# Performance work log

Measured on AMD Instinct MI355X. Metric: run time of the kernel, lower is better.

The kernel has to match this reference:

```python
import jax, jax.numpy as jnp
import numpy as np

N, E, H, L, T = 20000, 160000, 128, 4, 20


def _ln(x, g, b):
    m = jnp.mean(x, -1, keepdims=True)
    v = jnp.mean((x - m) ** 2, -1, keepdims=True)
    return (x - m) * jax.lax.rsqrt(v + 1e-5) * g + b


def _mlp(x, W1, b1, W2, b2, g, b):
    # Linear -> ReLU -> Linear -> LayerNorm, as in mlp_2layer
    h = jax.nn.relu(x @ W1 + b1)
    return _ln(h @ W2 + b2, g, b)


def setup_inputs() -> dict:
    key = jax.random.key(0)
    ks = iter(jax.random.split(key, 64))

    def W(shape):
        fan_in = shape[-2]
        return jax.random.normal(next(ks), shape, jnp.float32) * (fan_in ** -0.5)

    z = lambda s: jnp.zeros(s, jnp.float32)
    o = lambda s: jnp.ones(s, jnp.float32)

    inp = {
        'x': jax.random.normal(next(ks), (N, 12), jnp.float32),
        'edge_attr': jax.random.normal(next(ks), (E, 4), jnp.float32),
        'edge_index': jax.random.randint(next(ks), (2, E), 0, N),
        # node encoder (12 -> H)
        'Wn1': W((12, H)), 'bn1': z((H,)), 'Wn2': W((H, H)), 'bn2': z((H,)), 'gn_ln': o((H,)), 'bn_ln': z((H,)),
        # edge encoder (4 -> H)
        'We1': W((4, H)), 'be1': z((H,)), 'We2': W((H, H)), 'be2': z((H,)), 'ge_ln': o((H,)), 'be_ln': z((H,)),
        # stacked per-layer params: edge_mlp (4H -> H), node_mlp (3H -> H), global_mlp (3H -> H)
        'lEW1': W((L, 4 * H, H)), 'lEb1': z((L, H)), 'lEW2': W((L, H, H)), 'lEb2': z((L, H)), 'lEg': o((L, H)), 'lEbt': z((L, H)),
        'lVW1': W((L, 3 * H, H)), 'lVb1': z((L, H)), 'lVW2': W((L, H, H)), 'lVb2': z((L, H)), 'lVg': o((L, H)), 'lVbt': z((L, H)),
        'lGW1': W((L, 3 * H, H)), 'lGb1': z((L, H)), 'lGW2': W((L, H, H)), 'lGb2': z((L, H)), 'lGg': o((L, H)), 'lGbt': z((L, H)),
        # CNN output head: Conv1d(1->8,k=15,s=4) -> ReLU -> Conv1d(8->1,k=10,s=1)
        'c1w': jax.random.normal(next(ks), (8, 1, 15), jnp.float32) * 0.1, 'c1b': z((8,)),
        'c2w': jax.random.normal(next(ks), (1, 8, 10), jnp.float32) * 0.1, 'c2b': z((1,)),
    }
    return inp


def _forward(x, edge_attr, edge_index,
             Wn1, bn1, Wn2, bn2, gn_ln, bn_ln,
             We1, be1, We2, be2, ge_ln, be_ln,
             lEW1, lEb1, lEW2, lEb2, lEg, lEbt,
             lVW1, lVb1, lVW2, lVb2, lVg, lVbt,
             lGW1, lGb1, lGW2, lGb2, lGg, lGbt,
             c1w, c1b, c2w, c2b):
    senders = edge_index[0]
    receivers = edge_index[1]
    n_nodes = x.shape[0]
    n_edges = edge_attr.shape[0]

    x_v = _mlp(x, Wn1, bn1, Wn2, bn2, gn_ln, bn_ln)          # [N, H]
    x_e = _mlp(edge_attr, We1, be1, We2, be2, ge_ln, be_ln)  # [E, H]
    g = jnp.zeros((1, H), x_v.dtype)                          # B=1 global (no global inputs)

    def step(carry, p):
        x_v, x_e, g = carry
        (EW1, Eb1, EW2, Eb2, Eg, Ebt,
         VW1, Vb1, VW2, Vb2, Vg, Vbt,
         GW1, Gb1, GW2, Gb2, Gg, Gbt) = p
        # edge update: gather sender/receiver feats, concat with edge + global
        g_e = jnp.broadcast_to(g, (n_edges, H))
        edge_in = jnp.concatenate([x_v[senders], x_v[receivers], x_e, g_e], -1)  # [E, 4H]
        x_e = x_e + _mlp(edge_in, EW1, Eb1, EW2, Eb2, Eg, Ebt)
        # node update: sum-aggregate messages by receiver
        aggr = jax.ops.segment_sum(x_e, receivers, num_segments=n_nodes)  # [N, H]
        g_v = jnp.broadcast_to(g, (n_nodes, H))
        node_in = jnp.concatenate([x_v, aggr, g_v], -1)  # [N, 3H]
        x_v = x_v + _mlp(node_in, VW1, Vb1, VW2, Vb2, Vg, Vbt)
        # global update
        g_in = jnp.concatenate([jnp.sum(x_v, 0, keepdims=True), jnp.sum(x_e, 0, keepdims=True), g], -1)  # [1, 3H]
        g = g + _mlp(g_in, GW1, Gb1, GW2, Gb2, Gg, Gbt)
        return (x_v, x_e, g), None

    params = (lEW1, lEb1, lEW2, lEb2, lEg, lEbt,
              lVW1, lVb1, lVW2, lVb2, lVg, lVbt,
              lGW1, lGb1, lGW2, lGb2, lGg, lGbt)
    (x_v, x_e, g), _ = jax.lax.scan(step, (x_v, x_e, g), params)

    # CNN head over the H=128 feature axis -> [N, T]
    dn = ('NCH', 'OIH', 'NCH')
    h = x_v[:, None, :]  # [N, 1, 128]
    h = jax.lax.conv_general_dilated(h, c1w, (4,), 'VALID', dimension_numbers=dn)
    h = jax.nn.relu(h + c1b[None, :, None])  # [N, 8, 29]
    h = jax.lax.conv_general_dilated(h, c2w, (1,), 'VALID', dimension_numbers=dn) + c2b[None, :, None]
    return h[:, 0, :]  # [N, 20]


def reference(x, edge_attr, edge_index,
              Wn1, bn1, Wn2, bn2, gn_ln, bn_ln,
              We1, be1, We2, be2, ge_ln, be_ln,
              lEW1, lEb1, lEW2, lEb2, lEg, lEbt,
              lVW1, lVb1, lVW2, lVb2, lVg, lVbt,
              lGW1, lGb1, lGW2, lGb2, lGg, lGbt,
              c1w, c1b, c2w, c2b):
    return _forward(x, edge_attr, edge_index,
                    Wn1, bn1, Wn2, bn2, gn_ln, bn_ln,
                    We1, be1, We2, be2, ge_ln, be_ln,
                    lEW1, lEb1, lEW2, lEb2, lEg, lEbt,
                    lVW1, lVb1, lVW2, lVb2, lVg, lVbt,
                    lGW1, lGb1, lGW2, lGb2, lGg, lGbt,
                    c1w, c1b, c2w, c2b)
```

## Files before the change

### kernel.cpp

```cpp
#include <hip/hip_runtime.h>

#define NN 20000
#define NE 160000
#define HD 128
#define SA 136

typedef __attribute__((ext_vector_type(8))) short  bfrag;
typedef __attribute__((ext_vector_type(4))) short  s4v;
typedef __attribute__((ext_vector_type(4))) float  facc;
typedef __attribute__((ext_vector_type(4))) float  f4v;

__device__ __forceinline__ float bf2f(unsigned short u){
  union { unsigned int i; float f; } v; v.i = ((unsigned int)u) << 16; return v.f;
}
__device__ __forceinline__ unsigned short f2bf(float f){
  union { float f; unsigned int i; } v; v.f = f;
  unsigned int r = v.i + 0x7fffu + ((v.i >> 16) & 1u);
  return (unsigned short)(r >> 16);
}

__global__ void sentinel_kernel(float* out, float code){
  if (threadIdx.x < 32) out[threadIdx.x] = code;
}

__device__ __forceinline__ void gemm_tile(const short* Ab,
                                          const unsigned short* pk,
                                          int m0, int lane, facc acc[8]){
  const int q = lane >> 4, c = lane & 15;
  #pragma unroll
  for (int kt = 0; kt < 4; ++kt){
    bfrag a = *(const bfrag*)(Ab + (m0 + c) * SA + kt * 32 + q * 8);
    const bfrag* bp = (const bfrag*)pk + kt * 512 + lane;
    #pragma unroll
    for (int nt = 0; nt < 8; ++nt){
      acc[nt] = __builtin_amdgcn_mfma_f32_16x16x32_bf16(a, bp[nt * 64], acc[nt], 0, 0, 0);
    }
  }
}

__device__ __forceinline__ void gemm_tile_h(const short* Ab,
                                            const unsigned short* pk,
                                            int m0, int ntb, int lane, facc acc[4]){
  const int q = lane >> 4, c = lane & 15;
  #pragma unroll
  for (int kt = 0; kt < 4; ++kt){
    bfrag a = *(const bfrag*)(Ab + (m0 + c) * SA + kt * 32 + q * 8);
    const bfrag* bp = (const bfrag*)pk + kt * 512 + ntb * 64 + lane;
    #pragma unroll
    for (int nt = 0; nt < 4; ++nt){
      acc[nt] = __builtin_amdgcn_mfma_f32_16x16x32_bf16(a, bp[nt * 64], acc[nt], 0, 0, 0);
    }
  }
}

__global__ __launch_bounds__(256) void pack_all(
    const float* Wn2, const float* We2,
    const float* lEW1, const float* lEW2,
    const float* lVW1, const float* lVW2,
    unsigned short* packed)
{
  int job = blockIdx.x * 256 + threadIdx.x;
  int mat = job >> 12, r12 = job & 4095;
  int plane = r12 >> 11, r = r12 & 2047;
  int kt = r >> 9, nt = (r >> 6) & 7, lane = r & 63;
  const float* src;
  if (mat == 0) src = Wn2;
  else if (mat == 1) src = We2;
  else {
    int m2 = mat - 2, l = m2 / 7, t = m2 % 7;
    switch (t){
      case 0: src = lEW1 + ((size_t)l*512 +   0)*HD; break;
      case 1: src = lEW1 + ((size_t)l*512 + 128)*HD; break;
      case 2: src = lEW1 + ((size_t)l*512 + 256)*HD; break;
      case 3: src = lEW2 + (size_t)l*HD*HD;          break;
      case 4: src = lVW1 + ((size_t)l*384 +   0)*HD; break;
      case 5: src = lVW1 + ((size_t)l*384 + 128)*HD; break;
      default: src = lVW2 + (size_t)l*HD*HD;         break;
    }
  }
  int krow = kt*32 + (lane>>4)*8, col = nt*16 + (lane&15);
  unsigned short v[8];
  #pragma unroll
  for (int j = 0; j < 8; ++j){
    float w = src[(size_t)(krow + j)*HD + col];
    unsigned short h = f2bf(w);
    v[j] = plane ? f2bf(w - bf2f(h)) : h;
  }
  unsigned short* dst = packed + ((size_t)mat*2 + plane)*16384
                               + ((size_t)(kt*8+nt)*64 + lane)*8;
  #pragma unroll
  for (int j = 0; j < 8; ++j) dst[j] = v[j];
}

__global__ __launch_bounds__(128) void init_small(
    float* g, float* cbe, float* cbv, float* xvs, float* xes,
    const float* Eb1_0, const float* Vb1_0)
{
  int t = threadIdx.x;
  g[t] = 0.f; xvs[t] = 0.f; xes[t] = 0.f;
  cbe[t] = Eb1_0[t]; cbv[t] = Vb1_0[t];
}

__global__ __launch_bounds__(256) void zero_cnt(int* cnt){
  int i = blockIdx.x * 256 + threadIdx.x;
  if (i < NN) cnt[i] = 0;
}
__global__ __launch_bounds__(256) void hist_kernel(const int* eidx, int* cnt){
  int e = blockIdx.x * 256 + threadIdx.x;
  atomicAdd(&cnt[eidx[NE + e]], 1);
}
__global__ __launch_bounds__(1024) void scan_kernel(const int* cnt, int* base, int* ofs){
  __shared__ int wsum[16];
  int t = threadIdx.x, lane = t & 63;
  int vals[20]; int loc = 0;
  if (t < 1000){
    #pragma unroll
    for (int k = 0; k < 20; ++k){ vals[k] = cnt[t*20 + k]; loc += vals[k]; }
  }
  int inc = loc;
  #pragma unroll
  for (int d = 1; d < 64; d <<= 1){ int o = __shfl_up(inc, d); if (lane >= d) inc += o; }
  if (lane == 63) wsum[t >> 6] = inc;
  __syncthreads();
  if (t < 16){
    int v = wsum[t];
    #pragma unroll
    for (int d = 1; d < 16; d <<= 1){ int o = __shfl_up(v, d); if (t >= d) v += o; }
    wsum[t] = v;
  }
  __syncthreads();
  int woff = (t >= 64) ? wsum[(t >> 6) - 1] : 0;
  int run = woff + inc - loc;
  if (t < 1000){
    #pragma unroll
    for (int k = 0; k < 20; ++k){ base[t*20 + k] = run; ofs[t*20 + k] = run; run += vals[k]; }
  }
  if (t == 0) base[NN] = NE;
}
__global__ __launch_bounds__(256) void scatter_kernel(const int* eidx, int* ofs,
                                                      int* perm, int* ssid, int* srid){
  int e = blockIdx.x * 256 + threadIdx.x;
  int s = eidx[e], r = eidx[NE + e];
  int pos = atomicAdd(&ofs[r], 1);
  perm[pos] = e; ssid[pos] = s; srid[pos] = r;
}

__global__ __launch_bounds__(256) void enc_node(
    const float* x, const float* W1, const float* b1,
    const unsigned short* pkW2, const float* b2,
    const float* gl, const float* bl, float* xvf, int nrows)
{
  __shared__ float inb[64*12];
  __shared__ __align__(16) short Hh[64*SA];
  __shared__ __align__(16) short Hl[64*SA];
  int tid = threadIdx.x, r0 = blockIdx.x * 64;
  for (int j = tid; j < 64*12; j += 256){
    int rr = j / 12, k = j % 12, rg = r0 + rr;
    inb[j] = (rg < nrows) ? x[(size_t)rg*12 + k] : 0.f;
  }
  __syncthreads();
  {
    int cc = tid & 127;
    float w1c[12];
    #pragma unroll
    for (int k = 0; k < 12; ++k) w1c[k] = W1[k*HD + cc];
    float bb = b1[cc];
    for (int it = 0; it < 32; ++it){
      int rr = it*2 + (tid >> 7);
      float a = bb;
      #pragma unroll
      for (int k = 0; k < 12; ++k) a += inb[rr*12 + k] * w1c[k];
      float h = fmaxf(a, 0.f);
      unsigned short hh = f2bf(h);
      Hh[rr*SA + cc] = (short)hh;
      Hl[rr*SA + cc] = (short)f2bf(h - bf2f(hh));
    }
  }
  __syncthreads();
  int lane = tid & 63, q = lane >> 4, c = lane & 15, m0 = (tid >> 6) * 16;
  facc a2[8];
  #pragma unroll
  for (int nt = 0; nt < 8; ++nt) a2[nt] = (facc){0.f,0.f,0.f,0.f};
  gemm_tile(Hh, pkW2,         m0, lane, a2);
  gemm_tile(Hl, pkW2,         m0, lane, a2);
  gemm_tile(Hh, pkW2 + 16384, m0, lane, a2);
  #pragma unroll
  for (int i = 0; i < 4; ++i){
    int rl = m0 + q*4 + i, rg = r0 + rl;
    float vals[8], s = 0.f, ss = 0.f;
    #pragma unroll
    for (int nt = 0; nt < 8; ++nt){
      float v = a2[nt][i] + b2[nt*16 + c];
      vals[nt] = v; s += v; ss += v*v;
    }
    s += __shfl_xor(s,1); ss += __shfl_xor(ss,1);
    s += __shfl_xor(s,2); ss += __shfl_xor(ss,2);
    s += __shfl_xor(s,4); ss += __shfl_xor(ss,4);
    s += __shfl_xor(s,8); ss += __shfl_xor(ss,8);
    float mean = s * 0.0078125f;
    float var  = ss * 0.0078125f - mean*mean;
    float rs   = rsqrtf(var + 1e-5f);
    if (rg < nrows){
      #pragma unroll
      for (int nt = 0; nt < 8; ++nt){
        int col = nt*16 + c;
        xvf[(size_t)rg*HD + col] = (vals[nt]-mean)*rs*gl[col] + bl[col];
      }
    }
  }
}

__global__ __launch_bounds__(256) void enc_edge(
    const float* ea, const int* perm, const float* W1, const float* b1,
    const unsigned short* pkW2, const float* b2,
    const float* gl, const float* bl, unsigned short* xeb)
{
  __shared__ float inb[64*4];
  __shared__ __align__(16) short Hh[64*SA];
  __shared__ __align__(16) short Hl[64*SA];
  int tid = threadIdx.x, r0 = blockIdx.x * 64;
  {
    int rr = tid >> 2, k = tid & 3;
    int pe = perm[r0 + rr];
    inb[tid] = ea[(size_t)pe*4 + k];
  }
  __syncthreads();
  {
    int cc = tid & 127;
    float w0 = W1[0*HD+cc], w1 = W1[1*HD+cc], w2 = W1[2*HD+cc], w3 = W1[3*HD+cc];
    float bb = b1[cc];
    for (int it = 0; it < 32; ++it){
      int rr = it*2 + (tid >> 7);
      float a = bb + inb[rr*4+0]*w0 + inb[rr*4+1]*w1 + inb[rr*4+2]*w2 + inb[rr*4+3]*w3;
      float h = fmaxf(a, 0.f);
      unsigned short hh = f2bf(h);
      Hh[rr*SA + cc] = (short)hh;
      Hl[rr*SA + cc] = (short)f2bf(h - bf2f(hh));
    }
  }
  __syncthreads();
  int lane = tid & 63, q = lane >> 4, c = lane & 15, m0 = (tid >> 6) * 16;
  facc a2[8];
  #pragma unroll
  for (int nt = 0; nt < 8; ++nt) a2[nt] = (facc){0.f,0.f,0.f,0.f};
  gemm_tile(Hh, pkW2,         m0, lane, a2);
  gemm_tile(Hl, pkW2,         m0, lane, a2);
  gemm_tile(Hh, pkW2 + 16384, m0, lane, a2);
  #pragma unroll
  for (int i = 0; i < 4; ++i){
    int rl = m0 + q*4 + i, rg = r0 + rl;
    float vals[8], s = 0.f, ss = 0.f;
    #pragma unroll
    for (int nt = 0; nt < 8; ++nt){
      float v = a2[nt][i] + b2[nt*16 + c];
      vals[nt] = v; s += v; ss += v*v;
    }
    s += __shfl_xor(s,1); ss += __shfl_xor(ss,1);
    s += __shfl_xor(s,2); ss += __shfl_xor(ss,2);
    s += __shfl_xor(s,4); ss += __shfl_xor(ss,4);
    s += __shfl_xor(s,8); ss += __shfl_xor(ss,8);
    float mean = s * 0.0078125f;
    float var  = ss * 0.0078125f - mean*mean;
    float rs   = rsqrtf(var + 1e-5f);
    #pragma unroll
    for (int nt = 0; nt < 8; ++nt){
      int col = nt*16 + c;
      xeb[(size_t)rg*HD + col] = f2bf((vals[nt]-mean)*rs*gl[col] + bl[col]);
    }
  }
}

__global__ __launch_bounds__(512, 4) void pq_kernel(
    const float* xvf, const unsigned short* pkA, const unsigned short* pkB,
    unsigned short* P, unsigned short* Q, int nrows)
{
  __shared__ __align__(16) short Ah[64*SA];
  __shared__ __align__(16) short Al[64*SA];
  int tid = threadIdx.x, r0 = blockIdx.x * 64;
  for (int j = tid; j < 1024; j += 512){
    int rr = j >> 4, ch = j & 15, rg = r0 + rr;
    float v[8];
    if (rg < nrows){
      f4v a = *(const f4v*)(xvf + (size_t)rg*HD + ch*8);
      f4v b = *(const f4v*)(xvf + (size_t)rg*HD + ch*8 + 4);
      v[0]=a[0];v[1]=a[1];v[2]=a[2];v[3]=a[3];v[4]=b[0];v[5]=b[1];v[6]=b[2];v[7]=b[3];
    } else {
      #pragma unroll
      for (int k = 0; k < 8; ++k) v[k] = 0.f;
    }
    short* dh = Ah + rr*SA + ch*8;
    short* dl = Al + rr*SA + ch*8;
    #pragma unroll
    for (int k = 0; k < 8; ++k){
      unsigned short h = f2bf(v[k]);
      dh[k] = (short)h; dl[k] = (short)f2bf(v[k] - bf2f(h));
    }
  }
  __syncthreads();
  int lane = tid & 63, wq = tid >> 6, q = lane >> 4, c = lane & 15;
  int m0 = (wq & 3) * 16, ntb = (wq >> 2) * 4;
  facc ap[4], aq[4];
  #pragma unroll
  for (int nt = 0; nt < 4; ++nt){ ap[nt] = (facc){0.f,0.f,0.f,0.f}; aq[nt] = (facc){0.f,0.f,0.f,0.f}; }
  gemm_tile_h(Ah, pkA,         m0, ntb, lane, ap);
  gemm_tile_h(Al, pkA,         m0, ntb, lane, ap);
  gemm_tile_h(Ah, pkA + 16384, m0, ntb, lane, ap);
  gemm_tile_h(Ah, pkB,         m0, ntb, lane, aq);
  gemm_tile_h(Al, pkB,         m0, ntb, lane, aq);
  gemm_tile_h(Ah, pkB + 16384, m0, ntb, lane, aq);
  #pragma unroll
  for (int i = 0; i < 4; ++i){
    int rl = m0 + q*4 + i, rg = r0 + rl;
    if (rg < nrows){
      s4v pv, qv;
      #pragma unroll
      for (int nt = 0; nt < 4; ++nt){
        pv[nt] = (short)f2bf(ap[nt][i]);
        qv[nt] = (short)f2bf(aq[nt][i]);
      }
      *(s4v*)(P + (size_t)rg*HD + c*8 + ntb) = pv;
      *(s4v*)(Q + (size_t)rg*HD + c*8 + ntb) = qv;
    }
  }
}

__global__ __launch_bounds__(512, 4) void edge_kernel(
    unsigned short* xeb, const int* ssid, const int* srid,
    const unsigned short* P, const unsigned short* Q, const float* cbe,
    const unsigned short* pkW1c, const unsigned short* pkW2,
    const float* Eb2, const float* Eg, const float* Ebt)
{
  __shared__ __align__(16) short Ab[64*SA];
  __shared__ __align__(16) short Hl[64*SA];
  __shared__ int sidx[64], ridx[64];
  __shared__ float lnS[128], lnSS[128];
  int tid = threadIdx.x, e0 = blockIdx.x * 64;
  for (int j = tid; j < 1024; j += 512){
    int rr = j >> 4, ch = j & 15;
    *(bfrag*)(Ab + rr*SA + ch*8) = *(const bfrag*)(xeb + (size_t)(e0+rr)*HD + ch*8);
  }
  if (tid < 64){ sidx[tid] = ssid[e0+tid]; ridx[tid] = srid[e0+tid]; }
  __syncthreads();
  int lane = tid & 63, wq = tid >> 6, q = lane >> 4, c = lane & 15;
  int m0 = (wq & 3) * 16, ntb = (wq >> 2) * 4, half = wq >> 2;
  unsigned int rres[4][2];
  #pragma unroll
  for (int i = 0; i < 4; ++i){
    int rl = m0 + q*4 + i;
    #pragma unroll
    for (int p2 = 0; p2 < 2; ++p2){
      unsigned short a0 = (unsigned short)Ab[rl*SA + (ntb + 2*p2    )*16 + c];
      unsigned short a1 = (unsigned short)Ab[rl*SA + (ntb + 2*p2 + 1)*16 + c];
      rres[i][p2] = ((unsigned int)a1 << 16) | a0;
    }
  }
  float cb[4];
  #pragma unroll
  for (int nt = 0; nt < 4; ++nt) cb[nt] = cbe[(ntb + nt)*16 + c];
  float pg[4][4];
  #pragma unroll
  for (int i = 0; i < 4; ++i){
    int rl = m0 + q*4 + i;
    s4v ps = *(const s4v*)(P + (size_t)sidx[rl]*HD + c*8 + ntb);
    s4v qr = *(const s4v*)(Q + (size_t)ridx[rl]*HD + c*8 + ntb);
    #pragma unroll
    for (int nt = 0; nt < 4; ++nt)
      pg[i][nt] = bf2f((unsigned short)ps[nt]) + bf2f((unsigned short)qr[nt]) + cb[nt];
  }
  facc acc[4];
  #pragma unroll
  for (int nt = 0; nt < 4; ++nt) acc[nt] = (facc){0.f,0.f,0.f,0.f};
  gemm_tile_h(Ab, pkW1c,         m0, ntb, lane, acc);
  gemm_tile_h(Ab, pkW1c + 16384, m0, ntb, lane, acc);
  __syncthreads();
  #pragma unroll
  for (int i = 0; i < 4; ++i){
    int rl = m0 + q*4 + i;
    #pragma unroll
    for (int nt = 0; nt < 4; ++nt){
      int col = (ntb + nt)*16 + c;
      float h = fmaxf(acc[nt][i] + pg[i][nt], 0.f);
      unsigned short hh = f2bf(h);
      Ab[rl*SA + col] = (short)hh;
      Hl[rl*SA + col] = (short)f2bf(h - bf2f(hh));
    }
  }
  __syncthreads();
  facc a2[4];
  #pragma unroll
  for (int nt = 0; nt < 4; ++nt) a2[nt] = (facc){0.f,0.f,0.f,0.f};
  gemm_tile_h(Ab, pkW2,         m0, ntb, lane, a2);
  gemm_tile_h(Hl, pkW2,         m0, ntb, lane, a2);
  gemm_tile_h(Ab, pkW2 + 16384, m0, ntb, lane, a2);
  float vals[4][4], myS[4], mySS[4];
  #pragma unroll
  for (int i = 0; i < 4; ++i){
    int rl = m0 + q*4 + i;
    float s = 0.f, ss = 0.f;
    #pragma unroll
    for (int nt = 0; nt < 4; ++nt){
      float v = a2[nt][i] + Eb2[(ntb + nt)*16 + c];
      vals[i][nt] = v; s += v; ss += v*v;
    }
    s += __shfl_xor(s,1); ss += __shfl_xor(ss,1);
    s += __shfl_xor(s,2); ss += __shfl_xor(ss,2);
    s += __shfl_xor(s,4); ss += __shfl_xor(ss,4);
    s += __shfl_xor(s,8); ss += __shfl_xor(ss,8);
    myS[i] = s; mySS[i] = ss;
    if (c == 0){ lnS[rl*2 + half] = s; lnSS[rl*2 + half] = ss; }
  }
  __syncthreads();
  #pragma unroll
  for (int i = 0; i < 4; ++i){
    int rl = m0 + q*4 + i, eg = e0 + rl;
    float sT  = myS[i]  + lnS[rl*2 + (half^1)];
    float ssT = mySS[i] + lnSS[rl*2 + (half^1)];
    float mean = sT * 0.0078125f;
    float var  = ssT * 0.0078125f - mean*mean;
    float rs   = rsqrtf(var + 1e-5f);
    #pragma unroll
    for (int nt = 0; nt < 4; ++nt){
      int col = (ntb + nt)*16 + c;
      float o = (vals[i][nt]-mean)*rs*Eg[col] + Ebt[col];
      float rv = bf2f((unsigned short)(rres[i][nt >> 1] >> ((nt & 1)*16)));
      xeb[(size_t)eg*HD + col] = f2bf(rv + o);
    }
  }
}

__global__ __launch_bounds__(512, 4) void node_kernel(
    float* xvf, const unsigned short* xeb, const int* base, const float* cbv,
    const unsigned short* pkW1a, const unsigned short* pkW1b, const unsigned short* pkW2,
    const float* Vb2, const float* Vg, const float* Vbt,
    float* xv_sum, float* xes, int do_xes, int nrows)
{
  __shared__ __align__(16) short Avh[64*SA];
  __shared__ __align__(16) short Avl[64*SA];
  __shared__ __align__(16) short Agh[64*SA];
  __shared__ __align__(16) short Agl[64*SA];
  __shared__ float red[128];
  __shared__ float lnS[128], lnSS[128];
  int tid = threadIdx.x, r0 = blockIdx.x * 64;
  int lane = tid & 63, wq = tid >> 6;
  if (tid < 128) red[tid] = 0.f;
  __syncthreads();
  for (int j = tid; j < 1024; j += 512){
    int rr = j >> 4, ch = j & 15, rg = r0 + rr;
    float v[8];
    if (rg < nrows){
      f4v a = *(const f4v*)(xvf + (size_t)rg*HD + ch*8);
      f4v b = *(const f4v*)(xvf + (size_t)rg*HD + ch*8 + 4);
      v[0]=a[0];v[1]=a[1];v[2]=a[2];v[3]=a[3];v[4]=b[0];v[5]=b[1];v[6]=b[2];v[7]=b[3];
    } else {
      #pragma unroll
      for (int k = 0; k < 8; ++k) v[k] = 0.f;
    }
    short *dvh = Avh + rr*SA + ch*8, *dvl = Avl + rr*SA + ch*8;
    #pragma unroll
    for (int k = 0; k < 8; ++k){
      unsigned short h1 = f2bf(v[k]);
      dvh[k] = (short)h1; dvl[k] = (short)f2bf(v[k] - bf2f(h1));
    }
  }
  float xp0 = 0.f, xp1 = 0.f;
  for (int j = 0; j < 8; ++j){
    int rl = wq*8 + j, rg = r0 + rl;
    float s0 = 0.f, s1 = 0.f;
    if (rg < nrows){
      int b0 = base[rg], b1 = base[rg + 1];
      int e = b0;
      for (; e + 1 < b1; e += 2){
        unsigned int u0 = *(const unsigned int*)(xeb + (size_t)e*HD + lane*2);
        unsigned int u1 = *(const unsigned int*)(xeb + (size_t)(e+1)*HD + lane*2);
        s0 += bf2f((unsigned short)(u0 & 0xffffu)) + bf2f((unsigned short)(u1 & 0xffffu));
        s1 += bf2f((unsigned short)(u0 >> 16))     + bf2f((unsigned short)(u1 >> 16));
      }
      if (e < b1){
        unsigned int u0 = *(const unsigned int*)(xeb + (size_t)e*HD + lane*2);
        s0 += bf2f((unsigned short)(u0 & 0xffffu));
        s1 += bf2f((unsigned short)(u0 >> 16));
      }
    }
    unsigned short h0 = f2bf(s0), h1 = f2bf(s1);
    unsigned short l0 = f2bf(s0 - bf2f(h0)), l1 = f2bf(s1 - bf2f(h1));
    *(unsigned int*)(Agh + rl*SA + 2*lane) = ((unsigned int)h1 << 16) | h0;
    *(unsigned int*)(Agl + rl*SA + 2*lane) = ((unsigned int)l1 << 16) | l0;
    xp0 += s0; xp1 += s1;
  }
  if (do_xes){
    atomicAdd(&red[lane*2],     xp0);
    atomicAdd(&red[lane*2 + 1], xp1);
  }
  __syncthreads();
  if (do_xes && tid < 128) atomicAdd(&xes[tid], red[tid]);
  int q = lane >> 4, c = lane & 15;
  int m0 = (wq & 3) * 16, ntb = (wq >> 2) * 4, half = wq >> 2;
  facc acc[4];
  #pragma unroll
  for (int nt = 0; nt < 4; ++nt) acc[nt] = (facc){0.f,0.f,0.f,0.f};
  gemm_tile_h(Avh, pkW1a,         m0, ntb, lane, acc);
  gemm_tile_h(Avl, pkW1a,         m0, ntb, lane, acc);
  gemm_tile_h(Avh, pkW1a + 16384, m0, ntb, lane, acc);
  gemm_tile_h(Agh, pkW1b,         m0, ntb, lane, acc);
  gemm_tile_h(Agl, pkW1b,         m0, ntb, lane, acc);
  gemm_tile_h(Agh, pkW1b + 16384, m0, ntb, lane, acc);
  __syncthreads();
  #pragma unroll
  for (int i = 0; i < 4; ++i){
    int rl = m0 + q*4 + i;
    #pragma unroll
    for (int nt = 0; nt < 4; ++nt){
      int col = (ntb + nt)*16 + c;
      float h = fmaxf(acc[nt][i] + cbv[col], 0.f);
      unsigned short hh = f2bf(h);
      Avh[rl*SA + col] = (short)hh;
      Avl[rl*SA + col] = (short)f2bf(h - bf2f(hh));
    }
  }
  __syncthreads();
  facc a2[4];
  #pragma unroll
  for (int nt = 0; nt < 4; ++nt) a2[nt] = (facc){0.f,0.f,0.f,0.f};
  gemm_tile_h(Avh, pkW2,         m0, ntb, lane, a2);
  gemm_tile_h(Avl, pkW2,         m0, ntb, lane, a2);
  gemm_tile_h(Avh, pkW2 + 16384, m0, ntb, lane, a2);
  float vals[4][4], myS[4], mySS[4];
  #pragma unroll
  for (int i = 0; i < 4; ++i){
    int rl = m0 + q*4 + i;
    float s = 0.f, ss = 0.f;
    #pragma unroll
    for (int nt = 0; nt < 4; ++nt){
      float v = a2[nt][i] + Vb2[(ntb + nt)*16 + c];
      vals[i][nt] = v; s += v; ss += v*v;
    }
    s += __shfl_xor(s,1); ss += __shfl_xor(ss,1);
    s += __shfl_xor(s,2); ss += __shfl_xor(ss,2);
    s += __shfl_xor(s,4); ss += __shfl_xor(ss,4);
    s += __shfl_xor(s,8); ss += __shfl_xor(ss,8);
    myS[i] = s; mySS[i] = ss;
    if (c == 0){ lnS[rl*2 + half] = s; lnSS[rl*2 + half] = ss; }
  }
  __syncthreads();
  float csum[4] = {0.f,0.f,0.f,0.f};
  #pragma unroll
  for (int i = 0; i < 4; ++i){
    int rl = m0 + q*4 + i, rg = r0 + rl;
    float sT  = myS[i]  + lnS[rl*2 + (half^1)];
    float ssT = mySS[i] + lnSS[rl*2 + (half^1)];
    float mean = sT * 0.0078125f;
    float var  = ssT * 0.0078125f - mean*mean;
    float rs   = rsqrtf(var + 1e-5f);
    if (rg < nrows){
      #pragma unroll
      for (int nt = 0; nt < 4; ++nt){
        int col = (ntb + nt)*16 + c;
        float o = (vals[i][nt]-mean)*rs*Vg[col] + Vbt[col];
        size_t gi = (size_t)rg*HD + col;
        float nv = xvf[gi] + o;
        xvf[gi] = nv;
        csum[nt] += nv;
      }
    }
  }
  #pragma unroll
  for (int nt = 0; nt < 4; ++nt){
    float v = csum[nt]; v += __shfl_xor(v,16); v += __shfl_xor(v,32);
    if (q == 0) atomicAdd(&xv_sum[(ntb + nt)*16 + c], v);
  }
}

__global__ __launch_bounds__(1024) void g_kernel(
    float* xvs, float* xes, float* g,
    const float* GW1, const float* Gb1, const float* GW2, const float* Gb2,
    const float* Gg, const float* Gbt,
    float* cbe, float* cbv,
    const float* EW1n, const float* Eb1n, const float* VW1n, const float* Vb1n)
{
  __shared__ float gin[384], h1[128], gn[128], red[4];
  __shared__ float partA[8][128], partB[8][128];
  int tid = threadIdx.x, t = tid & 127, kk = tid >> 7;
  if (tid < 384) gin[tid] = (tid < 128) ? xvs[tid] : (tid < 256) ? xes[tid-128] : g[tid-256];
  __syncthreads();
  {
    float a = 0.f;
    for (int k = kk*48; k < kk*48 + 48; ++k) a += gin[k] * GW1[(size_t)k*HD + t];
    partA[kk][t] = a;
  }
  __syncthreads();
  if (kk == 0){
    float a = Gb1[t];
    #pragma unroll
    for (int i = 0; i < 8; ++i) a += partA[i][t];
    h1[t] = fmaxf(a, 0.f);
  }
  __syncthreads();
  {
    float o = 0.f;
    for (int k = kk*16; k < kk*16 + 16; ++k) o += h1[k] * GW2[(size_t)k*HD + t];
    partA[kk][t] = o;
  }
  __syncthreads();
  float oo = 0.f;
  if (kk == 0){
    oo = Gb2[t];
    #pragma unroll
    for (int i = 0; i < 8; ++i) oo += partA[i][t];
  }
  __syncthreads();
  if (tid < 128){
    float s = oo;
    #pragma unroll
    for (int d = 1; d < 64; d <<= 1) s += __shfl_xor(s, d);
    if ((tid & 63) == 0) red[tid >> 6] = s;
  }
  __syncthreads();
  float mean = (red[0] + red[1]) * 0.0078125f;
  if (tid < 128){
    float dd = oo - mean;
    float v = dd * dd;
    #pragma unroll
    for (int d = 1; d < 64; d <<= 1) v += __shfl_xor(v, d);
    if ((tid & 63) == 0) red[2 + (tid >> 6)] = v;
  }
  __syncthreads();
  if (tid < 128){
    float rs = rsqrtf((red[2] + red[3]) * 0.0078125f + 1e-5f);
    float gnv = g[tid] + (oo - mean)*rs*Gg[tid] + Gbt[tid];
    g[tid] = gnv; gn[tid] = gnv;
    xvs[tid] = 0.f; xes[tid] = 0.f;
  }
  __syncthreads();
  {
    float ce = 0.f, cv = 0.f;
    for (int k = kk*16; k < kk*16 + 16; ++k){
      ce += gn[k] * EW1n[(size_t)k*HD + t];
      cv += gn[k] * VW1n[(size_t)k*HD + t];
    }
    partA[kk][t] = ce; partB[kk][t] = cv;
  }
  __syncthreads();
  if (kk == 0){
    float ce = Eb1n[t], cv = Vb1n[t];
    #pragma unroll
    for (int i = 0; i < 8; ++i){ ce += partA[i][t]; cv += partB[i][t]; }
    cbe[t] = ce; cbv[t] = cv;
  }
}

__global__ __launch_bounds__(256) void decoder_kernel(
    const float* xv, const float* c1w, const float* c1b,
    const float* c2w, const float* c2b, float* out)
{
  __shared__ float xl[4][128];
  __shared__ float hl[4][232];
  __shared__ float w1[120], b1[8], w2[80];
  __shared__ float b2s;
  int tid = threadIdx.x, nl = tid >> 6, t = tid & 63;
  int n = blockIdx.x * 4 + nl;
  if (tid < 120) w1[tid] = c1w[tid];
  else if (tid < 128) b1[tid - 120] = c1b[tid - 120];
  else if (tid < 208) w2[tid - 128] = c2w[tid - 128];
  else if (tid == 208) b2s = c2b[0];
  xl[nl][t]      = xv[(size_t)n*HD + t];
  xl[nl][t + 64] = xv[(size_t)n*HD + 64 + t];
  __syncthreads();
  for (int j = t; j < 232; j += 64){
    int ch = j / 29, pp = j % 29;
    float a = b1[ch];
    #pragma unroll
    for (int u = 0; u < 15; ++u) a += xl[nl][4*pp + u] * w1[ch*15 + u];
    hl[nl][j] = fmaxf(a, 0.f);
  }
  __syncthreads();
  if (t < 20){
    float o = b2s;
    #pragma unroll
    for (int ch = 0; ch < 8; ++ch)
      #pragma unroll
      for (int u = 0; u < 10; ++u)
        o += hl[nl][ch*29 + t + u] * w2[ch*10 + u];
    out[(size_t)n*20 + t] = o;
  }
}

extern "C" void kernel_launch(void* const* d_in, const int* in_sizes, int n_in,
                              void* d_out, int out_size, void* d_ws, size_t ws_size,
                              hipStream_t stream)
{
  const float* x    = (const float*)d_in[0];
  const float* ea   = (const float*)d_in[1];
  const int*   eidx = (const int*)d_in[2];
  const float* Wn1  = (const float*)d_in[3];  const float* bn1  = (const float*)d_in[4];
  const float* Wn2  = (const float*)d_in[5];  const float* bn2  = (const float*)d_in[6];
  const float* gnln = (const float*)d_in[7];  const float* bnln = (const float*)d_in[8];
  const float* We1  = (const float*)d_in[9];  const float* be1  = (const float*)d_in[10];
  const float* We2  = (const float*)d_in[11]; const float* be2  = (const float*)d_in[12];
  const float* geln = (const float*)d_in[13]; const float* beln = (const float*)d_in[14];
  const float* lEW1 = (const float*)d_in[15]; const float* lEb1 = (const float*)d_in[16];
  const float* lEW2 = (const float*)d_in[17]; const float* lEb2 = (const float*)d_in[18];
  const float* lEg  = (const float*)d_in[19]; const float* lEbt = (const float*)d_in[20];
  const float* lVW1 = (const float*)d_in[21]; const float* lVb1 = (const float*)d_in[22];
  const float* lVW2 = (const float*)d_in[23]; const float* lVb2 = (const float*)d_in[24];
  const float* lVg  = (const float*)d_in[25]; const float* lVbt = (const float*)d_in[26];
  const float* lGW1 = (const float*)d_in[27]; const float* lGb1 = (const float*)d_in[28];
  const float* lGW2 = (const float*)d_in[29]; const float* lGb2 = (const float*)d_in[30];
  const float* lGg  = (const float*)d_in[31]; const float* lGbt = (const float*)d_in[32];
  const float* c1w  = (const float*)d_in[33]; const float* c1b  = (const float*)d_in[34];
  const float* c2w  = (const float*)d_in[35]; const float* c2b  = (const float*)d_in[36];

  char* ws = (char*)d_ws;
  size_t off = 0;
  auto alloc = [&](size_t b){ size_t o = off; off += (b + 255) & ~(size_t)255; return o; };
  unsigned short* pk   = (unsigned short*)(ws + alloc((size_t)30*2*16384*2));
  float*          g    = (float*)(ws + alloc(512));
  float*          cbe  = (float*)(ws + alloc(512));
  float*          cbv  = (float*)(ws + alloc(512));
  float*          xvs  = (float*)(ws + alloc(512));
  float*          xes  = (float*)(ws + alloc(512));
  float*          xvf  = (float*)(ws + alloc((size_t)NN*HD*4));
  unsigned short* P    = (unsigned short*)(ws + alloc((size_t)NN*HD*2));
  unsigned short* Q    = (unsigned short*)(ws + alloc((size_t)NN*HD*2));
  unsigned short* xeb  = (unsigned short*)(ws + alloc((size_t)NE*HD*2));
  int*            cnt  = (int*)(ws + alloc((size_t)NN*4));
  int*            bse  = (int*)(ws + alloc((size_t)(NN+1)*4));
  int*            ofs  = (int*)(ws + alloc((size_t)NN*4));
  int*            perm = (int*)(ws + alloc((size_t)NE*4));
  int*            ssid = (int*)(ws + alloc((size_t)NE*4));
  int*            srid = (int*)(ws + alloc((size_t)NE*4));

  if (ws_size < off){
    sentinel_kernel<<<1, 32, 0, stream>>>((float*)d_out, 20000.f + (float)(ws_size >> 20));
    return;
  }

  auto slot = [&](int m){ return pk + (size_t)m * 32768; };

  pack_all<<<480, 256, 0, stream>>>(Wn2, We2, lEW1, lEW2, lVW1, lVW2, pk);
  init_small<<<1, 128, 0, stream>>>(g, cbe, cbv, xvs, xes, lEb1, lVb1);
  zero_cnt<<<(NN + 255)/256, 256, 0, stream>>>(cnt);
  hist_kernel<<<NE/256, 256, 0, stream>>>(eidx, cnt);
  scan_kernel<<<1, 1024, 0, stream>>>(cnt, bse, ofs);
  scatter_kernel<<<NE/256, 256, 0, stream>>>(eidx, ofs, perm, ssid, srid);

  enc_node<<<(NN + 63)/64, 256, 0, stream>>>(x, Wn1, bn1, slot(0), bn2, gnln, bnln, xvf, NN);
  enc_edge<<<NE/64, 256, 0, stream>>>(ea, perm, We1, be1, slot(1), be2, geln, beln, xeb);

  for (int l = 0; l < 4; ++l){
    int m = 2 + 7*l;
    pq_kernel<<<(NN + 63)/64, 512, 0, stream>>>(xvf, slot(m+0), slot(m+1), P, Q, NN);
    edge_kernel<<<NE/64, 512, 0, stream>>>(xeb, ssid, srid, P, Q, cbe,
        slot(m+2), slot(m+3),
        lEb2 + (size_t)l*HD, lEg + (size_t)l*HD, lEbt + (size_t)l*HD);
    node_kernel<<<(NN + 63)/64, 512, 0, stream>>>(xvf, xeb, bse, cbv,
        slot(m+4), slot(m+5), slot(m+6),
        lVb2 + (size_t)l*HD, lVg + (size_t)l*HD, lVbt + (size_t)l*HD,
        xvs, xes, (l < 3) ? 1 : 0, NN);
    if (l < 3){
      g_kernel<<<1, 1024, 0, stream>>>(xvs, xes, g,
          lGW1 + (size_t)l*384*HD, lGb1 + (size_t)l*HD,
          lGW2 + (size_t)l*HD*HD, lGb2 + (size_t)l*HD,
          lGg + (size_t)l*HD, lGbt + (size_t)l*HD,
          cbe, cbv,
          lEW1 + ((size_t)(l+1)*512 + 384)*HD, lEb1 + (size_t)(l+1)*HD,
          lVW1 + ((size_t)(l+1)*384 + 256)*HD, lVb1 + (size_t)(l+1)*HD);
    }
  }
  decoder_kernel<<<NN/4, 256, 0, stream>>>(xvf, c1w, c1b, c2w, c2b, (float*)d_out);

  hipError_t e = hipGetLastError();
  if (e != hipSuccess){
    sentinel_kernel<<<1, 32, 0, stream>>>((float*)d_out, 10000.f + (float)e);
  }
  (void)in_sizes; (void)n_in; (void)out_size;
}
```

Measured before the change: 833.4 us.

## Fuse next-layer P/Q projection into node kernel and prefetch edge gathers early

The node kernel now computes the next layer's P and Q projections from the freshly updated node features it already holds in shared memory. This removes three of the four per-layer pq_kernel launches and the re-read of xvf they needed. Only the first pq_kernel stays, before the layer loop. Separately, the edge kernel loads its sender/receiver indices into registers and issues the P/Q gathers before the xeb tile load, so those gather latencies overlap. The cost is higher register and shared-memory pressure in both kernels and a longer node kernel.

After: 832.7 us. Within noise of the previous version (-0.1%).

```diff
diff --git a/kernel.cpp b/kernel.cpp
--- a/kernel.cpp
+++ b/kernel.cpp
@@ -332,17 +332,31 @@
 {
   __shared__ __align__(16) short Ab[64*SA];
   __shared__ __align__(16) short Hl[64*SA];
-  __shared__ int sidx[64], ridx[64];
   __shared__ float lnS[128], lnSS[128];
   int tid = threadIdx.x, e0 = blockIdx.x * 64;
+  int lane = tid & 63, wq = tid >> 6, q = lane >> 4, c = lane & 15;
+  int m0 = (wq & 3) * 16, ntb = (wq >> 2) * 4, half = wq >> 2;
+
+  int sid[4], rid[4];
+  #pragma unroll
+  for (int i = 0; i < 4; ++i){
+    int rl = m0 + q*4 + i;
+    sid[i] = ssid[e0 + rl];
+    rid[i] = srid[e0 + rl];
+  }
+  s4v psv[4], qrv[4];
+  #pragma unroll
+  for (int i = 0; i < 4; ++i){
+    psv[i] = *(const s4v*)(P + (size_t)sid[i]*HD + c*8 + ntb);
+    qrv[i] = *(const s4v*)(Q + (size_t)rid[i]*HD + c*8 + ntb);
+  }
+
   for (int j = tid; j < 1024; j += 512){
     int rr = j >> 4, ch = j & 15;
     *(bfrag*)(Ab + rr*SA + ch*8) = *(const bfrag*)(xeb + (size_t)(e0+rr)*HD + ch*8);
   }
-  if (tid < 64){ sidx[tid] = ssid[e0+tid]; ridx[tid] = srid[e0+tid]; }
-  __syncthreads();
-  int lane = tid & 63, wq = tid >> 6, q = lane >> 4, c = lane & 15;
-  int m0 = (wq & 3) * 16, ntb = (wq >> 2) * 4, half = wq >> 2;
+  __syncthreads();
+
   unsigned int rres[4][2];
   #pragma unroll
   for (int i = 0; i < 4; ++i){
@@ -360,12 +374,9 @@
   float pg[4][4];
   #pragma unroll
   for (int i = 0; i < 4; ++i){
-    int rl = m0 + q*4 + i;
-    s4v ps = *(const s4v*)(P + (size_t)sidx[rl]*HD + c*8 + ntb);
-    s4v qr = *(const s4v*)(Q + (size_t)ridx[rl]*HD + c*8 + ntb);
     #pragma unroll
     for (int nt = 0; nt < 4; ++nt)
-      pg[i][nt] = bf2f((unsigned short)ps[nt]) + bf2f((unsigned short)qr[nt]) + cb[nt];
+      pg[i][nt] = bf2f((unsigned short)psv[i][nt]) + bf2f((unsigned short)qrv[i][nt]) + cb[nt];
   }
   facc acc[4];
   #pragma unroll
@@ -432,7 +443,9 @@
     float* xvf, const unsigned short* xeb, const int* base, const float* cbv,
     const unsigned short* pkW1a, const unsigned short* pkW1b, const unsigned short* pkW2,
     const float* Vb2, const float* Vg, const float* Vbt,
-    float* xv_sum, float* xes, int do_xes, int nrows)
+    float* xv_sum, float* xes, int do_xes,
+    const unsigned short* pkAn, const unsigned short* pkBn,
+    unsigned short* P, unsigned short* Q, int do_pq, int nrows)
 {
   __shared__ __align__(16) short Avh[64*SA];
   __shared__ __align__(16) short Avl[64*SA];
@@ -560,6 +573,11 @@
         float nv = xvf[gi] + o;
         xvf[gi] = nv;
         csum[nt] += nv;
+        if (do_pq){
+          unsigned short hh = f2bf(nv);
+          Agh[rl*SA + col] = (short)hh;
+          Agl[rl*SA + col] = (short)f2bf(nv - bf2f(hh));
+        }
       }
     }
   }
@@ -567,6 +585,32 @@
   for (int nt = 0; nt < 4; ++nt){
     float v = csum[nt]; v += __shfl_xor(v,16); v += __shfl_xor(v,32);
     if (q == 0) atomicAdd(&xv_sum[(ntb + nt)*16 + c], v);
+  }
+  if (do_pq){
+    __syncthreads();
+    facc ap[4], aq[4];
+    #pragma unroll
+    for (int nt = 0; nt < 4; ++nt){ ap[nt] = (facc){0.f,0.f,0.f,0.f}; aq[nt] = (facc){0.f,0.f,0.f,0.f}; }
+    gemm_tile_h(Agh, pkAn,         m0, ntb, lane, ap);
+    gemm_tile_h(Agl, pkAn,         m0, ntb, lane, ap);
+    gemm_tile_h(Agh, pkAn + 16384, m0, ntb, lane, ap);
+    gemm_tile_h(Agh, pkBn,         m0, ntb, lane, aq);
+    gemm_tile_h(Agl, pkBn,         m0, ntb, lane, aq);
+    gemm_tile_h(Agh, pkBn + 16384, m0, ntb, lane, aq);
+    #pragma unroll
+    for (int i = 0; i < 4; ++i){
+      int rl = m0 + q*4 + i, rg = r0 + rl;
+      if (rg < nrows){
+        s4v pv, qv;
+        #pragma unroll
+        for (int nt = 0; nt < 4; ++nt){
+          pv[nt] = (short)f2bf(ap[nt][i]);
+          qv[nt] = (short)f2bf(aq[nt][i]);
+        }
+        *(s4v*)(P + (size_t)rg*HD + c*8 + ntb) = pv;
+        *(s4v*)(Q + (size_t)rg*HD + c*8 + ntb) = qv;
+      }
+    }
   }
 }
 
@@ -746,16 +790,18 @@
   enc_node<<<(NN + 63)/64, 256, 0, stream>>>(x, Wn1, bn1, slot(0), bn2, gnln, bnln, xvf, NN);
   enc_edge<<<NE/64, 256, 0, stream>>>(ea, perm, We1, be1, slot(1), be2, geln, beln, xeb);
 
+  pq_kernel<<<(NN + 63)/64, 512, 0, stream>>>(xvf, slot(2), slot(3), P, Q, NN);
+
   for (int l = 0; l < 4; ++l){
     int m = 2 + 7*l;
-    pq_kernel<<<(NN + 63)/64, 512, 0, stream>>>(xvf, slot(m+0), slot(m+1), P, Q, NN);
     edge_kernel<<<NE/64, 512, 0, stream>>>(xeb, ssid, srid, P, Q, cbe,
         slot(m+2), slot(m+3),
         lEb2 + (size_t)l*HD, lEg + (size_t)l*HD, lEbt + (size_t)l*HD);
     node_kernel<<<(NN + 63)/64, 512, 0, stream>>>(xvf, xeb, bse, cbv,
         slot(m+4), slot(m+5), slot(m+6),
         lVb2 + (size_t)l*HD, lVg + (size_t)l*HD, lVbt + (size_t)l*HD,
-        xvs, xes, (l < 3) ? 1 : 0, NN);
+        xvs, xes, (l < 3) ? 1 : 0,
+        slot(m+7), slot(m+8), P, Q, (l < 3) ? 1 : 0, NN);
     if (l < 3){
       g_kernel<<<1, 1024, 0, stream>>>(xvs, xes, g,
           lGW1 + (size_t)l*384*HD, lGb1 + (size_t)l*HD,
```
